# Optimization experiments

Hardware: AMD Instinct MI355X
Metric: run time of the kernel (lower is better)

Reference implementation:

```python
import jax, jax.numpy as jnp
import numpy as np

K = 7          # kernel_size (square)
P = K // 2     # padding
NUM_HEADS = 12


def setup_inputs() -> dict:
    key = jax.random.key(0)
    ks = jax.random.split(key, 6)
    B, H, W, D = 16, 56, 56, 768
    x = jax.random.normal(ks[0], (B, H, W, D), jnp.float32)
    qkv_w = jax.random.normal(ks[1], (3 * D, D), jnp.float32) * 0.02
    qkv_b = jnp.zeros((3 * D,), jnp.float32)
    rel_bias = jax.random.normal(ks[2], (1, NUM_HEADS, 1, K * K), jnp.float32)
    proj_w = jax.random.normal(ks[3], (D, D), jnp.float32) * 0.02
    proj_b = jnp.zeros((D,), jnp.float32)
    return {"x": x, "qkv_w": qkv_w, "qkv_b": qkv_b, "rel_bias": rel_bias,
            "proj_w": proj_w, "proj_b": proj_b}


def reference(x, qkv_w, qkv_b, rel_bias, proj_w, proj_b):
    B, H, W, D = x.shape
    hd = D // NUM_HEADS
    scale = 1.0 / np.sqrt(hd)

    qkv = x @ qkv_w.T + qkv_b                       # [B,H,W,3D]
    qkv = jnp.pad(qkv, ((0, 0), (P, P), (P, P), (0, 0)))  # zero-pad spatially
    Hp, Wp = H + 2 * P, W + 2 * P
    qkv = qkv.reshape(B, Hp, Wp, 3, NUM_HEADS, hd)
    qkv = jnp.transpose(qkv, (3, 0, 4, 1, 2, 5))    # [3,B,nh,Hp,Wp,hd]
    qf, kf, vf = qkv[0], qkv[1], qkv[2]

    q = qf[:, :, P:P + H, P:P + W, :]               # [B,nh,H,W,hd] (center pixel queries)

    # validity of each padded position (out-of-bounds keys get -inf, matching the torch mask)
    valid = jnp.pad(jnp.ones((H, W), dtype=bool), ((P, P), (P, P)))

    # scores per kernel offset; offsets iterate row-major (di, dj) matching
    # torch.meshgrid(..., indexing='ij') flattening used for relative_position_bias
    scores = []
    for di in range(K):
        for dj in range(K):
            ksh = kf[:, :, di:di + H, dj:dj + W, :]           # shifted keys [B,nh,H,W,hd]
            s = jnp.einsum('bnhwd,bnhwd->bnhw', q, ksh) * scale
            s = s + rel_bias[0, :, 0, di * K + dj][None, :, None, None]
            vmask = valid[di:di + H, dj:dj + W]
            s = jnp.where(vmask[None, None, :, :], s, -jnp.inf)
            scores.append(s)
    scores = jnp.stack(scores, axis=-1)             # [B,nh,H,W,K*K]
    attn = jax.nn.softmax(scores, axis=-1)

    out = jnp.zeros_like(q)
    for di in range(K):
        for dj in range(K):
            vsh = vf[:, :, di:di + H, dj:dj + W, :]
            out = out + attn[..., di * K + dj, None] * vsh

    out = jnp.transpose(out, (0, 2, 3, 1, 4)).reshape(B, H, W, D)
    return out @ proj_w.T + proj_b
```

## Files before the change

### kernel.cpp

```cpp
#include <hip/hip_runtime.h>
#include <hip/hip_bf16.h>

typedef __attribute__((ext_vector_type(8))) short short8;
typedef __attribute__((ext_vector_type(4))) short s16x4;
typedef __attribute__((ext_vector_type(4))) float f32x4;

#define AS1 __attribute__((address_space(1)))
#define AS3 __attribute__((address_space(3)))

__device__ __forceinline__ void gld16(const short* g, short* l) {
  __builtin_amdgcn_global_load_lds((const AS1 void*)g, (AS3 void*)l, 16, 0, 0);
}

__device__ __forceinline__ float bf2f(short x) {
  return __uint_as_float(((unsigned)(unsigned short)x) << 16);
}
__device__ __forceinline__ short f2bf(float f) {
  unsigned u = __float_as_uint(f);
  return (short)((u + 0x7fffu + ((u >> 16) & 1u)) >> 16);
}
__device__ __forceinline__ short f2bfn(float f) {
  __hip_bfloat16 h = __float2bfloat16(f);
  return *reinterpret_cast<short*>(&h);
}

__global__ void cast_f32_bf16(const float* __restrict__ src, short* __restrict__ dst, int n8) {
  int stride = gridDim.x * blockDim.x;
  for (int i = blockIdx.x * blockDim.x + threadIdx.x; i < n8; i += stride) {
    const float4* s = (const float4*)(src + (size_t)i * 8);
    float4 a = s[0], b = s[1];
    short8 o;
    o[0] = f2bf(a.x); o[1] = f2bf(a.y); o[2] = f2bf(a.z); o[3] = f2bf(a.w);
    o[4] = f2bf(b.x); o[5] = f2bf(b.y); o[6] = f2bf(b.z); o[7] = f2bf(b.w);
    *(short8*)(dst + (size_t)i * 8) = o;
  }
}

template<int OUT_BF16>
__global__ __launch_bounds__(512, 2) void gemm256(
    const short* __restrict__ A, const short* __restrict__ Bm,
    const float* __restrict__ bias, void* __restrict__ C,
    int M, int N, int Kd, int NB)
{
  __shared__ short As[2][256 * 64];
  __shared__ short Bs[2][256 * 64];
  const int tid = threadIdx.x;
  const int wave = tid >> 6, lane = tid & 63;

  int nwg = gridDim.x;
  int q8 = nwg >> 3, r8 = nwg & 7;
  int xcd = blockIdx.x & 7, loc = blockIdx.x >> 3;
  int nb2 = (xcd < r8 ? xcd * (q8 + 1) : r8 * (q8 + 1) + (xcd - r8) * q8) + loc;
  int per = NB << 2;
  int sr = nb2 / per, rem = nb2 - sr * per;
  int nblk = rem >> 2, mrow = rem & 3;
  int mblk = sr * 4 + mrow;

  size_t arow0 = (size_t)mblk * 256;
  size_t brow0 = (size_t)nblk * 256;
  const int wm = wave >> 2, wn = wave & 3;
  const int lr = lane & 15, grp = lane >> 4;

  const short* gsa[4]; const short* gsb[4]; int sdst[4];
  #pragma unroll
  for (int i = 0; i < 4; ++i) {
    int f = i * 512 + tid;
    int row = f >> 3;
    int colc = (f & 7) ^ (row & 7);
    gsa[i] = A  + (arow0 + row) * Kd + colc * 8;
    gsb[i] = Bm + (brow0 + row) * Kd + colc * 8;
    sdst[i] = (i * 512 + wave * 64) * 8;
  }

  f32x4 acc[8][4];
  #pragma unroll
  for (int i = 0; i < 8; ++i)
    #pragma unroll
    for (int j = 0; j < 4; ++j) {
      acc[i][j][0] = 0.f; acc[i][j][1] = 0.f; acc[i][j][2] = 0.f; acc[i][j][3] = 0.f;
    }

  int aoff[8][2], boff[4][2];
  #pragma unroll
  for (int mi = 0; mi < 8; ++mi) {
    int arow = wm * 128 + mi * 16 + lr;
    #pragma unroll
    for (int kk = 0; kk < 2; ++kk) {
      int cb = kk * 64 + grp * 16;
      aoff[mi][kk] = arow * 64 + ((cb ^ ((arow & 7) << 4)) >> 1);
    }
  }
  #pragma unroll
  for (int nj = 0; nj < 4; ++nj) {
    int brow = wn * 64 + nj * 16 + lr;
    #pragma unroll
    for (int kk = 0; kk < 2; ++kk) {
      int cb = kk * 64 + grp * 16;
      boff[nj][kk] = brow * 64 + ((cb ^ ((brow & 7) << 4)) >> 1);
    }
  }

  const int NK = Kd >> 6;

  #pragma unroll
  for (int i = 0; i < 4; ++i) gld16(gsa[i], &As[0][sdst[i]]);
  #pragma unroll
  for (int i = 0; i < 4; ++i) gld16(gsb[i], &Bs[0][sdst[i]]);

  int cur = 0;
  for (int t = 0; t < NK; ++t) {
    if (t + 1 < NK) {
      int koff = (t + 1) << 6;
      #pragma unroll
      for (int i = 0; i < 4; ++i) gld16(gsa[i] + koff, &As[cur ^ 1][sdst[i]]);
      #pragma unroll
      for (int i = 0; i < 4; ++i) gld16(gsb[i] + koff, &Bs[cur ^ 1][sdst[i]]);
      asm volatile("s_waitcnt vmcnt(8)" ::: "memory");
    } else {
      asm volatile("s_waitcnt vmcnt(0)" ::: "memory");
    }
    __builtin_amdgcn_s_barrier();
    asm volatile("" ::: "memory");

    const short* pa = As[cur];
    const short* pb = Bs[cur];
    #pragma unroll
    for (int kk = 0; kk < 2; ++kk) {
      short8 bfr[4];
      #pragma unroll
      for (int nj = 0; nj < 4; ++nj) bfr[nj] = *(const short8*)&pb[boff[nj][kk]];
      #pragma unroll
      for (int mh = 0; mh < 2; ++mh) {
        short8 af[4];
        #pragma unroll
        for (int r = 0; r < 4; ++r) af[r] = *(const short8*)&pa[aoff[mh * 4 + r][kk]];
        __builtin_amdgcn_s_setprio(1);
        #pragma unroll
        for (int r = 0; r < 4; ++r)
          #pragma unroll
          for (int nj = 0; nj < 4; ++nj)
            acc[mh * 4 + r][nj] = __builtin_amdgcn_mfma_f32_16x16x32_bf16(
                af[r], bfr[nj], acc[mh * 4 + r][nj], 0, 0, 0);
        __builtin_amdgcn_s_setprio(0);
      }
    }
    asm volatile("" ::: "memory");
    __builtin_amdgcn_s_barrier();
    asm volatile("" ::: "memory");
    cur ^= 1;
  }

  int r0 = grp * 4;
  #pragma unroll
  for (int i = 0; i < 8; ++i) {
    size_t grow0 = arow0 + wm * 128 + i * 16 + r0;
    #pragma unroll
    for (int j = 0; j < 4; ++j) {
      size_t gcol = brow0 + wn * 64 + j * 16 + lr;
      float bv = bias[gcol];
      #pragma unroll
      for (int r = 0; r < 4; ++r) {
        float v = acc[i][j][r] + bv;
        size_t off = (grow0 + r) * (size_t)N + gcol;
        if (OUT_BF16) ((short*)C)[off] = f2bf(v);
        else          ((float*)C)[off] = v;
      }
    }
  }
}

__global__ void build_idx(unsigned char* __restrict__ idxt) {
  int tile = blockIdx.x;
  int ht = tile >> 2, wt = tile & 3;
  int tid = threadIdx.x;
  int wave = tid >> 6, lane = tid & 63;
  int grp = lane >> 4, q = lane & 15;
  int Sw = (22 * wave) & ~7;
  unsigned w[12];
  #pragma unroll
  for (int i = 0; i < 12; ++i) w[i] = 0x31313131u;
  #pragma unroll
  for (int kt = 0; kt < 10; ++kt) {
    unsigned wd = 0;
    #pragma unroll
    for (int r = 0; r < 4; ++r) {
      int i22 = Sw + kt * 16 + grp * 4 + r;
      int hr = i22 / 22, hc = i22 - hr * 22;
      int dr = hr - wave, dc = hc - q;
      int kh = ht * 4 - 3 + hr, kw = wt * 16 - 3 + hc;
      bool valid = ((unsigned)dr < 7u) && ((unsigned)dc < 7u) &&
                   ((unsigned)kh < 56u) && ((unsigned)kw < 56u);
      unsigned o = valid ? (unsigned)(dr * 7 + dc) : 49u;
      wd |= o << (r * 8);
    }
    w[kt] = wd;
  }
  uint4* dst = (uint4*)(idxt + (((size_t)tile * 4 + wave) * 64 + lane) * 48);
  dst[0] = make_uint4(w[0], w[1], w[2], w[3]);
  dst[1] = make_uint4(w[4], w[5], w[6], w[7]);
  dst[2] = make_uint4(w[8], w[9], w[10], w[11]);
}

#define HALO_V 232

__global__ __launch_bounds__(256, 4) void attn_mfma(
    const short* __restrict__ qkv, const float* __restrict__ rel_bias,
    const unsigned char* __restrict__ idxt, const short* __restrict__ zp,
    short* __restrict__ attn_out)
{
  __shared__ __align__(16) short kvbuf[HALO_V * 64];
  __shared__ float sbias[52];

  const int tid = threadIdx.x;
  const int wave = tid >> 6, lane = tid & 63;
  const int tile = blockIdx.x;
  const int ht = tile >> 2, wt = tile & 3;
  const int head = blockIdx.y % 12, b = blockIdx.y / 12;
  const int r0 = ht * 4, c0 = wt * 16;
  const int grp = lane >> 4, q = lane & 15;
  const int grp4 = grp * 4, grp8 = grp * 8;
  const int Sw = (22 * wave) & ~7;

  if (tid < 50) sbias[tid] = (tid < 49) ? rel_bias[head * 49 + tid] : -1e30f;

  const uint4* ip = (const uint4*)(idxt + (((size_t)tile * 4 + wave) * 64 + lane) * 48);
  uint4 iw0 = ip[0], iw1 = ip[1], iw2 = ip[2];
  unsigned idxw[10] = {iw0.x, iw0.y, iw0.z, iw0.w, iw1.x, iw1.y, iw1.z, iw1.w,
                       iw2.x, iw2.y};

  const int qrow = r0 + wave;
  const int qcol = min(c0 + q, 55);
  const short* qp = qkv + ((size_t)((b * 56 + qrow) * 56 + qcol)) * 2304 + head * 64;
  short8 qf0 = *(const short8*)(qp + grp8);
  short8 qf1 = *(const short8*)(qp + 32 + grp8);

  #pragma unroll
  for (int it = 0; it < 8; ++it) {
    int f = it * 256 + tid;
    if (f < HALO_V * 8) {
      int row = f >> 3, cc = f & 7;
      int hr = row / 22, hc = row - hr * 22;
      int gh = r0 - 3 + hr, gw = c0 - 3 + hc;
      bool ok = (row < 220) && ((unsigned)gh < 56u) && ((unsigned)gw < 56u);
      const short* src = ok
        ? qkv + ((size_t)((b * 56 + gh) * 56 + gw)) * 2304 + 768 + head * 64
              + ((cc ^ (row & 7)) * 8)
        : zp;
      gld16(src, &kvbuf[(it * 256 + wave * 64) * 8]);
    }
  }

  __syncthreads();

  short8 va[4], vb[4];
  int vq = 0, dcc = 0;
  const bool vact = (tid < HALO_V);
  if (vact) {
    vq = tid % 58; dcc = tid / 58;
    #pragma unroll
    for (int rr = 0; rr < 4; ++rr) {
      int vec = vq * 4 + rr;
      int hr = vec / 22, hc = vec - hr * 22;
      int gh = r0 - 3 + hr, gw = c0 - 3 + hc;
      bool ok = (vec < 220) && ((unsigned)gh < 56u) && ((unsigned)gw < 56u);
      const short8* vp = ok
        ? (const short8*)(qkv + ((size_t)((b * 56 + gh) * 56 + gw)) * 2304
                          + 1536 + head * 64 + dcc * 16)
        : (const short8*)zp;
      va[rr] = vp[0]; vb[rr] = vp[1];
    }
  }

  f32x4 accs[10];
  #pragma unroll
  for (int kt = 0; kt < 10; ++kt) {
    accs[kt][0] = 0.f; accs[kt][1] = 0.f; accs[kt][2] = 0.f; accs[kt][3] = 0.f;
  }
  #pragma unroll
  for (int kt = 0; kt < 10; ++kt) {
    int vec = Sw + kt * 16 + q;
    int sw = vec & 7;
    short8 k0 = *(const short8*)&kvbuf[vec * 64 + ((grp ^ sw)) * 8];
    short8 k1 = *(const short8*)&kvbuf[vec * 64 + (((grp + 4) ^ sw)) * 8];
    accs[kt] = __builtin_amdgcn_mfma_f32_16x16x32_bf16(k0, qf0, accs[kt], 0, 0, 0);
    accs[kt] = __builtin_amdgcn_mfma_f32_16x16x32_bf16(k1, qf1, accs[kt], 0, 0, 0);
  }

  __syncthreads();

  float mx = -1e30f;
  #pragma unroll
  for (int kt = 0; kt < 10; ++kt) {
    #pragma unroll
    for (int r = 0; r < 4; ++r) {
      float bia = sbias[(idxw[kt] >> (r * 8)) & 0xffu];
      float s = fmaf(accs[kt][r], 0.125f, bia);
      accs[kt][r] = s;
      mx = fmaxf(mx, s);
    }
  }
  mx = fmaxf(mx, __shfl_xor(mx, 16));
  mx = fmaxf(mx, __shfl_xor(mx, 32));
  float sum = 0.f;
  #pragma unroll
  for (int kt = 0; kt < 10; ++kt)
    #pragma unroll
    for (int r = 0; r < 4; ++r) {
      float e = __expf(accs[kt][r] - mx);
      accs[kt][r] = e;
      sum += e;
    }
  sum += __shfl_xor(sum, 16);
  sum += __shfl_xor(sum, 32);
  float inv = 1.0f / sum;

  if (vact) {
    #pragma unroll
    for (int dd = 0; dd < 8; ++dd) {
      s16x4 w;
      w[0] = va[0][dd]; w[1] = va[1][dd]; w[2] = va[2][dd]; w[3] = va[3][dd];
      *(s16x4*)&kvbuf[(dcc * 16 + dd) * HALO_V + vq * 4] = w;
    }
    #pragma unroll
    for (int dd = 0; dd < 8; ++dd) {
      s16x4 w;
      w[0] = vb[0][dd]; w[1] = vb[1][dd]; w[2] = vb[2][dd]; w[3] = vb[3][dd];
      *(s16x4*)&kvbuf[(dcc * 16 + 8 + dd) * HALO_V + vq * 4] = w;
    }
  }

  unsigned plo[10], phi[10];
  #pragma unroll
  for (int kt = 0; kt < 10; ++kt) {
    plo[kt] = (unsigned)(unsigned short)f2bfn(accs[kt][0])
            | ((unsigned)(unsigned short)f2bfn(accs[kt][1]) << 16);
    phi[kt] = (unsigned)(unsigned short)f2bfn(accs[kt][2])
            | ((unsigned)(unsigned short)f2bfn(accs[kt][3]) << 16);
  }

  __syncthreads();

  const int src0 = ((grp & 1) << 5) + q;
  const bool hi = (grp >> 1) & 1;
  f32x4 acco[4];
  #pragma unroll
  for (int dt = 0; dt < 4; ++dt) {
    acco[dt][0] = 0.f; acco[dt][1] = 0.f; acco[dt][2] = 0.f; acco[dt][3] = 0.f;
  }
  #pragma unroll
  for (int km = 0; km < 5; ++km) {
    int aw0 = __shfl((int)plo[2*km], src0),      bw0 = __shfl((int)plo[2*km+1], src0);
    int aw1 = __shfl((int)phi[2*km], src0),      bw1 = __shfl((int)phi[2*km+1], src0);
    int aw2 = __shfl((int)plo[2*km], src0 + 16), bw2 = __shfl((int)plo[2*km+1], src0 + 16);
    int aw3 = __shfl((int)phi[2*km], src0 + 16), bw3 = __shfl((int)phi[2*km+1], src0 + 16);
    int4 wv = make_int4(hi ? bw0 : aw0, hi ? bw1 : aw1,
                        hi ? bw2 : aw2, hi ? bw3 : aw3);
    short8 pf = *(short8*)&wv;
    #pragma unroll
    for (int dt = 0; dt < 4; ++dt) {
      short8 vf = *(const short8*)&kvbuf[(dt * 16 + q) * HALO_V + Sw + km * 32 + grp8];
      acco[dt] = __builtin_amdgcn_mfma_f32_16x16x32_bf16(pf, vf, acco[dt], 0, 0, 0);
    }
  }

  float invr[4];
  #pragma unroll
  for (int r = 0; r < 4; ++r) invr[r] = __shfl(inv, grp4 + r);
  #pragma unroll
  for (int dt = 0; dt < 4; ++dt) {
    #pragma unroll
    for (int r = 0; r < 4; ++r) {
      int qc = c0 + grp4 + r;
      if (qc < 56) {
        size_t off = ((size_t)((b * 56 + qrow) * 56 + qc)) * 768
                     + head * 64 + dt * 16 + q;
        attn_out[off] = f2bfn(acco[dt][r] * invr[r]);
      }
    }
  }
}

extern "C" void kernel_launch(void* const* d_in, const int* in_sizes, int n_in,
                              void* d_out, int out_size, void* d_ws, size_t ws_size,
                              hipStream_t stream)
{
  const float* x      = (const float*)d_in[0];
  const float* qkv_w  = (const float*)d_in[1];
  const float* qkv_b  = (const float*)d_in[2];
  const float* rel_b  = (const float*)d_in[3];
  const float* proj_w = (const float*)d_in[4];
  const float* proj_b = (const float*)d_in[5];

  char* ws = (char*)d_ws;
  short* x_bf    = (short*)(ws);
  short* attn_bf = (short*)(ws);
  short* qw_bf   = (short*)(ws + 77070336);
  short* pw_bf   = (short*)(ws + 80609280);
  short* qkv_bf  = (short*)(ws + 81788928);
  unsigned char* idxt = (unsigned char*)(ws + 312999936);
  short* zp      = (short*)(ws + 313688064);

  hipMemsetAsync(zp, 0, 256, stream);
  build_idx<<<56, 256, 0, stream>>>(idxt);

  cast_f32_bf16<<<2048, 256, 0, stream>>>(x, x_bf, 38535168 / 8);
  cast_f32_bf16<<<864, 256, 0, stream>>>(qkv_w, qw_bf, 1769472 / 8);
  cast_f32_bf16<<<288, 256, 0, stream>>>(proj_w, pw_bf, 589824 / 8);

  gemm256<1><<<1764, 512, 0, stream>>>(x_bf, qw_bf, qkv_b, (void*)qkv_bf,
                                       50176, 2304, 768, 9);

  attn_mfma<<<dim3(56, 192), 256, 0, stream>>>(qkv_bf, rel_b, idxt, zp, attn_bf);

  gemm256<0><<<588, 512, 0, stream>>>(attn_bf, pw_bf, proj_b, d_out,
                                      50176, 768, 768, 3);
}
```

Measured before the change: 483.6 us.

## Interleave next-tile global-to-LDS loads across four MFMA phases in GEMM loop

Restructures the GEMM main loop into four phases per K-tile. Each phase loads a slice of A fragments from LDS, issues part of the next tile's global_load_lds transfers, waits on a partial vmcnt, and then runs its MFMA group, with barriers placed between phases. The aim is to spread memory traffic across the compute and avoid one large load burst followed by a stall. In exchange it adds more barriers per iteration, and the correctness of the partial vmcnt counts depends on the order in which loads complete relative to the LDS reads.

After: 487.8 us. No clear change (+0.9%).

```diff
diff --git a/kernel.cpp b/kernel.cpp
--- a/kernel.cpp
+++ b/kernel.cpp
@@ -102,52 +102,81 @@
 
   const int NK = Kd >> 6;
 
-  #pragma unroll
-  for (int i = 0; i < 4; ++i) gld16(gsa[i], &As[0][sdst[i]]);
-  #pragma unroll
-  for (int i = 0; i < 4; ++i) gld16(gsb[i], &Bs[0][sdst[i]]);
-
-  int cur = 0;
+  gld16(gsa[0], &As[0][sdst[0]]);
+  gld16(gsa[2], &As[0][sdst[2]]);
+  gld16(gsb[0], &Bs[0][sdst[0]]);
+  gld16(gsb[1], &Bs[0][sdst[1]]);
+  gld16(gsb[2], &Bs[0][sdst[2]]);
+  gld16(gsb[3], &Bs[0][sdst[3]]);
+  gld16(gsa[1], &As[0][sdst[1]]);
+  gld16(gsa[3], &As[0][sdst[3]]);
+  asm volatile("s_waitcnt vmcnt(2)" ::: "memory");
+  __builtin_amdgcn_s_barrier();
+  asm volatile("" ::: "memory");
+
   for (int t = 0; t < NK; ++t) {
-    if (t + 1 < NK) {
-      int koff = (t + 1) << 6;
+    const short* pa = As[t & 1];
+    const short* pb = Bs[t & 1];
+    short* nA = As[(t + 1) & 1];
+    short* nB = Bs[(t + 1) & 1];
+    const int koff = (t + 1) << 6;
+    const bool more = (t + 1 < NK);
+
+    short8 bfr[4][2];
+    #pragma unroll
+    for (int p = 0; p < 4; ++p) {
+      short8 af[2][2];
       #pragma unroll
-      for (int i = 0; i < 4; ++i) gld16(gsa[i] + koff, &As[cur ^ 1][sdst[i]]);
+      for (int r = 0; r < 2; ++r)
+        #pragma unroll
+        for (int kk = 0; kk < 2; ++kk)
+          af[r][kk] = *(const short8*)&pa[aoff[2 * p + r][kk]];
+      if (p == 0) {
+        #pragma unroll
+        for (int nj = 0; nj < 4; ++nj)
+          #pragma unroll
+          for (int kk = 0; kk < 2; ++kk)
+            bfr[nj][kk] = *(const short8*)&pb[boff[nj][kk]];
+      }
+      if (more) {
+        if (p == 0) {
+          gld16(gsa[0] + koff, &nA[sdst[0]]);
+          gld16(gsa[2] + koff, &nA[sdst[2]]);
+          gld16(gsb[0] + koff, &nB[sdst[0]]);
+        } else if (p == 1) {
+          gld16(gsb[1] + koff, &nB[sdst[1]]);
+          gld16(gsb[2] + koff, &nB[sdst[2]]);
+          gld16(gsb[3] + koff, &nB[sdst[3]]);
+        } else if (p == 2) {
+          gld16(gsa[1] + koff, &nA[sdst[1]]);
+        } else {
+          gld16(gsa[3] + koff, &nA[sdst[3]]);
+        }
+      }
+      if (p == 1) {
+        if (more) asm volatile("s_waitcnt vmcnt(6)" ::: "memory");
+        else      asm volatile("s_waitcnt vmcnt(0)" ::: "memory");
+      }
+      if (p == 3 && more) asm volatile("s_waitcnt vmcnt(2)" ::: "memory");
+
+      asm volatile("" ::: "memory");
+      __builtin_amdgcn_s_barrier();
+      asm volatile("s_waitcnt lgkmcnt(0)" ::: "memory");
+      __builtin_amdgcn_sched_barrier(0);
+      __builtin_amdgcn_s_setprio(1);
       #pragma unroll
-      for (int i = 0; i < 4; ++i) gld16(gsb[i] + koff, &Bs[cur ^ 1][sdst[i]]);
-      asm volatile("s_waitcnt vmcnt(8)" ::: "memory");
-    } else {
-      asm volatile("s_waitcnt vmcnt(0)" ::: "memory");
-    }
-    __builtin_amdgcn_s_barrier();
-    asm volatile("" ::: "memory");
-
-    const short* pa = As[cur];
-    const short* pb = Bs[cur];
-    #pragma unroll
-    for (int kk = 0; kk < 2; ++kk) {
-      short8 bfr[4];
-      #pragma unroll
-      for (int nj = 0; nj < 4; ++nj) bfr[nj] = *(const short8*)&pb[boff[nj][kk]];
-      #pragma unroll
-      for (int mh = 0; mh < 2; ++mh) {
-        short8 af[4];
+      for (int kk = 0; kk < 2; ++kk)
         #pragma unroll
-        for (int r = 0; r < 4; ++r) af[r] = *(const short8*)&pa[aoff[mh * 4 + r][kk]];
-        __builtin_amdgcn_s_setprio(1);
-        #pragma unroll
-        for (int r = 0; r < 4; ++r)
+        for (int r = 0; r < 2; ++r)
           #pragma unroll
           for (int nj = 0; nj < 4; ++nj)
-            acc[mh * 4 + r][nj] = __builtin_amdgcn_mfma_f32_16x16x32_bf16(
-                af[r], bfr[nj], acc[mh * 4 + r][nj], 0, 0, 0);
-        __builtin_amdgcn_s_setprio(0);
-      }
-    }
-    asm volatile("" ::: "memory");
-    __builtin_amdgcn_s_barrier();
-    asm volatile("" ::: "memory");
-    cur ^= 1;
+            acc[2 * p + r][nj] = __builtin_amdgcn_mfma_f32_16x16x32_bf16(
+                af[r][kk], bfr[nj][kk], acc[2 * p + r][nj], 0, 0, 0);
+      __builtin_amdgcn_s_setprio(0);
+      asm volatile("" ::: "memory");
+      __builtin_amdgcn_s_barrier();
+      asm volatile("" ::: "memory");
+    }
   }
 
   int r0 = grp * 4;
```
